# Optimization experiments

Measured on AMD Instinct MI355X. Metric: run time of the kernel, lower is better.

## Reference

```python
import jax, jax.numpy as jnp
import numpy as np
import math

N, D, C = 1024, 512, 70722
M_MARGIN = 0.4
H_SCALE = 0.333
S_SCALE = 64.0
EPS = 0.001


def setup_inputs() -> dict:
    key = jax.random.key(0)
    k1, k2, k3 = jax.random.split(key, 3)
    x = jax.random.normal(k1, (N, D), dtype=jnp.float32)
    labels = jax.random.randint(k2, (N,), 0, C, dtype=jnp.int64)
    # weights ~ N(0, 0.01) as in nn.Parameter init
    weights = 0.01 * jax.random.normal(k3, (C, D), dtype=jnp.float32)
    return {"x": x, "labels": labels, "weights": weights}


def reference(x, labels, weights):
    # world_size == 1: all-gather is identity and all labels are local.
    x_norms = jnp.maximum(jnp.linalg.norm(x, axis=1, keepdims=True), 1e-8)  # [N,1]

    norm_emb = x / jnp.maximum(jnp.linalg.norm(x, axis=1, keepdims=True), 1e-12)
    norm_w = weights / jnp.maximum(jnp.linalg.norm(weights, axis=1, keepdims=True), 1e-12)
    cosine = jnp.clip(norm_emb @ norm_w.T, -1.0, 1.0)  # [N,C]

    # AdaFace adaptive margin scaler (detached norms; t_alpha=1 -> batch stats = current stats)
    safe_norms = jax.lax.stop_gradient(jnp.clip(x_norms, 0.001, 100.0))  # [N,1]
    batch_mean = jnp.mean(safe_norms)
    batch_std = jnp.std(safe_norms, ddof=1)  # torch .std() is unbiased
    margin_scaler = jnp.clip((safe_norms - batch_mean) / (batch_std + EPS) * H_SCALE, -1.0, 1.0)  # [N,1]

    g_angular = -M_MARGIN * margin_scaler           # [N,1]
    g_add = M_MARGIN + M_MARGIN * margin_scaler     # [N,1]

    onehot = jax.nn.one_hot(labels, C, dtype=cosine.dtype)  # [N,C]

    theta = jnp.arccos(cosine)
    theta_m = jnp.clip(theta + onehot * g_angular, EPS, math.pi - EPS)
    logits = (jnp.cos(theta_m) - onehot * g_add) * S_SCALE  # [N,C]

    logp = jax.nn.log_softmax(logits, axis=-1)
    loss = -jnp.mean(jnp.take_along_axis(logp, labels[:, None], axis=1))
    return loss
```

## Files before the change

### kernel.cpp

```cpp
#include <hip/hip_runtime.h>
#include <hip/hip_bf16.h>
#include <stdint.h>

#define DIM 512
#define NROWS 1024
#define NCLS 70722

typedef float floatx4 __attribute__((ext_vector_type(4)));

__device__ __forceinline__ unsigned pk4_fp8(float a, float b, float c, float d) {
    unsigned v = 0;
    v = __builtin_amdgcn_cvt_pk_fp8_f32(a, b, v, false);
    v = __builtin_amdgcn_cvt_pk_fp8_f32(c, d, v, true);
    return v;
}

__device__ __forceinline__ float wave_reduce_sum(float s) {
    #pragma unroll
    for (int m = 1; m < 64; m <<= 1) s += __shfl_xor(s, m);
    return s;
}

__global__ __launch_bounds__(256) void prep_kernel(
        const float* __restrict__ x, const float* __restrict__ W,
        const int* __restrict__ labels,
        uint8_t* __restrict__ An, uint8_t* __restrict__ Wn8,
        float* __restrict__ rownorm, float* __restrict__ coslab,
        float* __restrict__ rowsum) {
    int b = blockIdx.x;
    int wv = threadIdx.x >> 6, lane = threadIdx.x & 63;
    if (b < NROWS / 4) {
        if (threadIdx.x < 4) rowsum[b * 4 + threadIdx.x] = 0.0f;
        int row = b * 4 + wv;
        int lab = labels[row];
        const float4* xs = (const float4*)(x + (size_t)row * DIM);
        const float4* ws = (const float4*)(W + (size_t)lab * DIM);
        float4 xa = xs[lane * 2], xb = xs[lane * 2 + 1];
        float4 wa = ws[lane * 2], wb = ws[lane * 2 + 1];
        float dxx = xa.x*xa.x + xa.y*xa.y + xa.z*xa.z + xa.w*xa.w
                  + xb.x*xb.x + xb.y*xb.y + xb.z*xb.z + xb.w*xb.w;
        float dww = wa.x*wa.x + wa.y*wa.y + wa.z*wa.z + wa.w*wa.w
                  + wb.x*wb.x + wb.y*wb.y + wb.z*wb.z + wb.w*wb.w;
        float dxw = xa.x*wa.x + xa.y*wa.y + xa.z*wa.z + xa.w*wa.w
                  + xb.x*wb.x + xb.y*wb.y + xb.z*wb.z + xb.w*wb.w;
        dxx = wave_reduce_sum(dxx);
        dww = wave_reduce_sum(dww);
        dxw = wave_reduce_sum(dxw);
        float norm = sqrtf(dxx);
        float s16 = 16.0f / fmaxf(norm, 1e-12f);
        uint2 p;
        p.x = pk4_fp8(xa.x*s16, xa.y*s16, xa.z*s16, xa.w*s16);
        p.y = pk4_fp8(xb.x*s16, xb.y*s16, xb.z*s16, xb.w*s16);
        *(uint2*)(An + (size_t)row * DIM + lane * 8) = p;
        if (lane == 0) {
            rownorm[row] = norm;
            coslab[row]  = dxw / (fmaxf(norm, 1e-12f) * fmaxf(sqrtf(dww), 1e-12f));
        }
    } else {
        int c = (b - NROWS / 4) * 4 + wv;
        if (c < NCLS) {
            const float4* src = (const float4*)(W + (size_t)c * DIM);
            float4 va = src[lane * 2], vb = src[lane * 2 + 1];
            float ss = va.x*va.x + va.y*va.y + va.z*va.z + va.w*va.w
                     + vb.x*vb.x + vb.y*vb.y + vb.z*vb.z + vb.w*vb.w;
            ss = wave_reduce_sum(ss);
            float s16 = 16.0f / fmaxf(sqrtf(ss), 1e-12f);
            uint2 p;
            p.x = pk4_fp8(va.x*s16, va.y*s16, va.z*s16, va.w*s16);
            p.y = pk4_fp8(vb.x*s16, vb.y*s16, vb.z*s16, vb.w*s16);
            *(uint2*)(Wn8 + (size_t)c * DIM + lane * 8) = p;
        }
    }
}

__global__ __launch_bounds__(512, 2) void gemm6_kernel(
        const uint8_t* __restrict__ An, const uint8_t* __restrict__ Wn8,
        float* __restrict__ rowsum) {
    __shared__ uint8_t Asm[128 * 512];
    __shared__ uint8_t Bsm[2][256 * 128];
    __shared__ float red[128];

    int b = blockIdx.x;
    int mgrp = b >> 5, cgrp = b & 31;
    int tid = threadIdx.x, lane = tid & 63, wv = tid >> 6;
    if (tid < 128) red[tid] = 0.0f;

    int arow = tid >> 5;
    int aq = ((tid & 31) ^ (arow & 7)) * 16;
    const uint8_t* aGb = An + (size_t)(mgrp * 128 + arow) * DIM + aq;

    int brow = lane >> 3;
    int ckB = ((lane & 7) ^ brow) * 16;

    int wm = (wv >> 2) * 64, wn = (wv & 3) * 64;
    int fr = lane & 15, fq = lane >> 4;
    int fh = fq >> 1, fl = (fq & 1) * 8;

    const floatx4 vzero = {0.0f, 0.0f, 0.0f, 0.0f};
    floatx4 acc[4][4] = {};

#define GLL(gp, lp) __builtin_amdgcn_global_load_lds( \
        (const __attribute__((address_space(1))) unsigned int*)(gp), \
        (__attribute__((address_space(3))) unsigned int*)(lp), 16, 0, 0)
#define BAR  __builtin_amdgcn_s_barrier()
#define FEN  asm volatile("" ::: "memory")

    #pragma unroll
    for (int i = 0; i < 8; ++i)
        GLL(aGb + i * 8192, Asm + i * 8192 + wv * 1024);

    const uint8_t *bp0, *bp1, *bp2, *bp3;
    {
        int cb = cgrp * 256 + wv * 32 + brow;
        bp0 = Wn8 + (size_t)min(cb,      NCLS - 1) * DIM + ckB;
        bp1 = Wn8 + (size_t)min(cb + 8,  NCLS - 1) * DIM + ckB;
        bp2 = Wn8 + (size_t)min(cb + 16, NCLS - 1) * DIM + ckB;
        bp3 = Wn8 + (size_t)min(cb + 24, NCLS - 1) * DIM + ckB;
    }

#define STAGE_B(slot, kb) do { \
        uint8_t* _d = Bsm[slot] + wv * 4096; \
        GLL(bp0 + (kb), _d); \
        GLL(bp1 + (kb), _d + 1024); \
        GLL(bp2 + (kb), _d + 2048); \
        GLL(bp3 + (kb), _d + 3072); } while (0)

#define COMPUTE(slot, cA) do { \
        long af[4][4], bg[4][4]; \
        _Pragma("unroll") \
        for (int m = 0; m < 4; ++m) { \
            int R = wm + m * 16 + fr; \
            const uint8_t* rp = Asm + R * 512 + fl; \
            _Pragma("unroll") \
            for (int ks = 0; ks < 4; ++ks) { \
                int cch = (cA) + ks * 2 + fh; \
                af[m][ks] = *(const long*)(rp + ((cch ^ (R & 7)) * 16)); \
            } \
        } \
        _Pragma("unroll") \
        for (int n = 0; n < 4; ++n) { \
            int R = wn + n * 16 + fr; \
            const uint8_t* rp = Bsm[slot] + R * 128 + fl; \
            _Pragma("unroll") \
            for (int ks = 0; ks < 4; ++ks) { \
                int cch = ks * 2 + fh; \
                bg[n][ks] = *(const long*)(rp + ((cch ^ (R & 7)) * 16)); \
            } \
        } \
        _Pragma("unroll") \
        for (int ks = 0; ks < 4; ++ks) \
            _Pragma("unroll") \
            for (int m = 0; m < 4; ++m) \
                _Pragma("unroll") \
                for (int n = 0; n < 4; ++n) \
                    acc[m][n] = __builtin_amdgcn_mfma_f32_16x16x32_fp8_fp8( \
                        af[m][ks], bg[n][ks], acc[m][n], 0, 0, 0); \
    } while (0)

    STAGE_B(0, 0);

    int nct = (cgrp < 21) ? 9 : 8;
    int c = cgrp;
    for (int ct = 0; ct < nct; ++ct) {
        STAGE_B(1, 128);
        asm volatile("s_waitcnt vmcnt(4)" ::: "memory");
        BAR;
        COMPUTE(0, 0);
        FEN; BAR;
        STAGE_B(0, 256);
        asm volatile("s_waitcnt vmcnt(4)" ::: "memory");
        BAR;
        COMPUTE(1, 8);
        FEN; BAR;
        STAGE_B(1, 384);
        asm volatile("s_waitcnt vmcnt(4)" ::: "memory");
        BAR;
        COMPUTE(0, 16);
        FEN; BAR;
        if (ct != nct - 1) {
            int cb = (c + 32) * 256 + wv * 32 + brow;
            bp0 = Wn8 + (size_t)min(cb,      NCLS - 1) * DIM + ckB;
            bp1 = Wn8 + (size_t)min(cb + 8,  NCLS - 1) * DIM + ckB;
            bp2 = Wn8 + (size_t)min(cb + 16, NCLS - 1) * DIM + ckB;
            bp3 = Wn8 + (size_t)min(cb + 24, NCLS - 1) * DIM + ckB;
            STAGE_B(0, 0);
            asm volatile("s_waitcnt vmcnt(4)" ::: "memory");
        } else {
            asm volatile("s_waitcnt vmcnt(0)" ::: "memory");
        }
        BAR;
        COMPUTE(1, 24);
        FEN; BAR;

        {
            const float CLIPC = 0.99999950f;
            const float ISCL  = 1.0f / 256.0f;
            int colbase = c * 256 + wn + fr;
            #pragma unroll
            for (int m = 0; m < 4; ++m) {
                #pragma unroll
                for (int reg = 0; reg < 4; ++reg) {
                    float s = 0.0f;
                    #pragma unroll
                    for (int n = 0; n < 4; ++n) {
                        int col = colbase + n * 16;
                        float cc = acc[m][n][reg] * ISCL;
                        cc = fminf(fmaxf(cc, -CLIPC), CLIPC);
                        float term = __expf(64.0f * cc - 64.0f);
                        s += (col < NCLS) ? term : 0.0f;
                    }
                    s += __shfl_xor(s, 1); s += __shfl_xor(s, 2);
                    s += __shfl_xor(s, 4); s += __shfl_xor(s, 8);
                    if (fr == 0) atomicAdd(&red[wm + m * 16 + fq * 4 + reg], s);
                }
            }
            #pragma unroll
            for (int m = 0; m < 4; ++m)
                #pragma unroll
                for (int n = 0; n < 4; ++n)
                    acc[m][n] = vzero;
        }
        c += 32;
    }

#undef GLL
#undef STAGE_B
#undef COMPUTE
#undef BAR
#undef FEN

    __syncthreads();
    if (tid < 128) atomicAdd(rowsum + mgrp * 128 + tid, red[tid]);
}

__global__ __launch_bounds__(1024) void finalize_kernel(
        const float* __restrict__ rowsum, const float* __restrict__ coslab,
        const float* __restrict__ rownorm, float* __restrict__ out) {
    __shared__ float sd[1024];
    int t = threadIdx.x;
    float v = fminf(fmaxf(rownorm[t], 0.001f), 100.0f);
    sd[t] = v; __syncthreads();
    for (int s = 512; s > 0; s >>= 1) { if (t < s) sd[t] += sd[t + s]; __syncthreads(); }
    float mean = sd[0] * (1.0f / 1024.0f);
    __syncthreads();
    float d = v - mean;
    sd[t] = d * d; __syncthreads();
    for (int s = 512; s > 0; s >>= 1) { if (t < s) sd[t] += sd[t + s]; __syncthreads(); }
    float stdv = sqrtf(sd[0] * (1.0f / 1023.0f));
    float ms = d / (stdv + 0.001f) * 0.333f;
    ms = fminf(fmaxf(ms, -1.0f), 1.0f);
    float g_ang = -0.4f * ms;
    float g_add =  0.4f + 0.4f * ms;
    const float CLIPC = 0.99999950f;
    const float PI = 3.14159265358979323846f;
    float cl  = fminf(fmaxf(coslab[t], -1.0f), 1.0f);
    float cne = fminf(fmaxf(cl, -CLIPC), CLIPC);
    float logit_non = 64.0f * cne;
    float theta = acosf(cl);
    float tm = fminf(fmaxf(theta + g_ang, 0.001f), PI - 0.001f);
    float logit_true = (__cosf(tm) - g_add) * 64.0f;
    float ssum = rowsum[t] - __expf(logit_non - 64.0f) + __expf(logit_true - 64.0f);
    float loss = logf(ssum) + 64.0f - logit_true;
    __syncthreads();
    sd[t] = loss; __syncthreads();
    for (int s = 512; s > 0; s >>= 1) { if (t < s) sd[t] += sd[t + s]; __syncthreads(); }
    if (t == 0) out[0] = sd[0] * (1.0f / 1024.0f);
}

extern "C" void kernel_launch(void* const* d_in, const int* in_sizes, int n_in,
                              void* d_out, int out_size, void* d_ws, size_t ws_size,
                              hipStream_t stream) {
    const float* x      = (const float*)d_in[0];
    const int*   labels = (const int*)d_in[1];
    const float* W      = (const float*)d_in[2];
    float* out = (float*)d_out;
    char* ws = (char*)d_ws;

    const size_t SZ_WN8 = 36212736;
    const size_t SZ_AN  = 524288;
    uint8_t* Wn8 = (uint8_t*)ws;
    uint8_t* An  = (uint8_t*)(ws + SZ_WN8);
    float* rownorm = (float*)(ws + SZ_WN8 + SZ_AN);
    float* rowsum  = rownorm + 1024;
    float* coslab  = rowsum + 1024;

    int wblocks = (NCLS + 3) / 4;
    prep_kernel<<<NROWS / 4 + wblocks, 256, 0, stream>>>(
        x, W, labels, An, Wn8, rownorm, coslab, rowsum);
    gemm6_kernel<<<256, 512, 0, stream>>>(An, Wn8, rowsum);
    finalize_kernel<<<1, 1024, 0, stream>>>(rowsum, coslab, rownorm, out);
}
```

Baseline: 299.3 us.

## Hold A fragments in registers, defer row-sum reductions, add MFMA priority

The GEMM now loads every A-operand fragment for the wave's 64 rows once into registers (64 longs) rather than re-reading them from LDS in each K sub-step. The per-tile shuffle-and-atomic row reduction is replaced by per-thread running sums that are reduced once at the end. MFMA sections are wrapped in s_setprio to favour compute waves. The finalize kernel switches from a shared-memory tree reduction to wave shuffles. The larger register footprint risks spills or reduced occupancy under the 512x2 launch bound.

```diff
diff --git a/kernel.cpp b/kernel.cpp
--- a/kernel.cpp
+++ b/kernel.cpp
@@ -73,7 +73,7 @@
     }
 }
 
-__global__ __launch_bounds__(512, 2) void gemm6_kernel(
+__global__ __launch_bounds__(512, 2) void gemm7_kernel(
         const uint8_t* __restrict__ An, const uint8_t* __restrict__ Wn8,
         float* __restrict__ rowsum) {
     __shared__ uint8_t Asm[128 * 512];
@@ -98,6 +98,8 @@
 
     const floatx4 vzero = {0.0f, 0.0f, 0.0f, 0.0f};
     floatx4 acc[4][4] = {};
+    float srun[4][4] = {};
+    long af[4][16];
 
 #define GLL(gp, lp) __builtin_amdgcn_global_load_lds( \
         (const __attribute__((address_space(1))) unsigned int*)(gp), \
@@ -125,39 +127,36 @@
         GLL(bp2 + (kb), _d + 2048); \
         GLL(bp3 + (kb), _d + 3072); } while (0)
 
-#define COMPUTE(slot, cA) do { \
-        long af[4][4], bg[4][4]; \
-        _Pragma("unroll") \
-        for (int m = 0; m < 4; ++m) { \
-            int R = wm + m * 16 + fr; \
-            const uint8_t* rp = Asm + R * 512 + fl; \
-            _Pragma("unroll") \
-            for (int ks = 0; ks < 4; ++ks) { \
-                int cch = (cA) + ks * 2 + fh; \
-                af[m][ks] = *(const long*)(rp + ((cch ^ (R & 7)) * 16)); \
-            } \
-        } \
+    STAGE_B(0, 0);
+    asm volatile("s_waitcnt vmcnt(4)" ::: "memory");
+    BAR;
+
+    #pragma unroll
+    for (int m = 0; m < 4; ++m) {
+        int R = wm + m * 16 + fr;
+        const uint8_t* rp = Asm + R * 512 + fl;
+        #pragma unroll
+        for (int ksl = 0; ksl < 16; ++ksl)
+            af[m][ksl] = *(const long*)(rp + (((2 * ksl + fh) ^ (R & 7)) * 16));
+    }
+
+#define COMPUTE(slot, KSB) do { \
         _Pragma("unroll") \
         for (int n = 0; n < 4; ++n) { \
             int R = wn + n * 16 + fr; \
             const uint8_t* rp = Bsm[slot] + R * 128 + fl; \
+            long bg[4]; \
             _Pragma("unroll") \
-            for (int ks = 0; ks < 4; ++ks) { \
-                int cch = ks * 2 + fh; \
-                bg[n][ks] = *(const long*)(rp + ((cch ^ (R & 7)) * 16)); \
-            } \
+            for (int ks = 0; ks < 4; ++ks) \
+                bg[ks] = *(const long*)(rp + (((ks * 2 + fh) ^ (R & 7)) * 16)); \
+            _Pragma("unroll") \
+            for (int ks = 0; ks < 4; ++ks) \
+                _Pragma("unroll") \
+                for (int m = 0; m < 4; ++m) \
+                    acc[m][n] = __builtin_amdgcn_mfma_f32_16x16x32_fp8_fp8( \
+                        af[m][(KSB) + ks], bg[ks], acc[m][n], 0, 0, 0); \
         } \
-        _Pragma("unroll") \
-        for (int ks = 0; ks < 4; ++ks) \
-            _Pragma("unroll") \
-            for (int m = 0; m < 4; ++m) \
-                _Pragma("unroll") \
-                for (int n = 0; n < 4; ++n) \
-                    acc[m][n] = __builtin_amdgcn_mfma_f32_16x16x32_fp8_fp8( \
-                        af[m][ks], bg[n][ks], acc[m][n], 0, 0, 0); \
     } while (0)
-
-    STAGE_B(0, 0);
 
     int nct = (cgrp < 21) ? 9 : 8;
     int c = cgrp;
@@ -165,17 +164,17 @@
         STAGE_B(1, 128);
         asm volatile("s_waitcnt vmcnt(4)" ::: "memory");
         BAR;
-        COMPUTE(0, 0);
+        __builtin_amdgcn_s_setprio(1); COMPUTE(0, 0);  __builtin_amdgcn_s_setprio(0);
         FEN; BAR;
         STAGE_B(0, 256);
         asm volatile("s_waitcnt vmcnt(4)" ::: "memory");
         BAR;
-        COMPUTE(1, 8);
+        __builtin_amdgcn_s_setprio(1); COMPUTE(1, 4);  __builtin_amdgcn_s_setprio(0);
         FEN; BAR;
         STAGE_B(1, 384);
         asm volatile("s_waitcnt vmcnt(4)" ::: "memory");
         BAR;
-        COMPUTE(0, 16);
+        __builtin_amdgcn_s_setprio(1); COMPUTE(0, 8);  __builtin_amdgcn_s_setprio(0);
         FEN; BAR;
         if (ct != nct - 1) {
             int cb = (c + 32) * 256 + wv * 32 + brow;
@@ -189,7 +188,7 @@
             asm volatile("s_waitcnt vmcnt(0)" ::: "memory");
         }
         BAR;
-        COMPUTE(1, 24);
+        __builtin_amdgcn_s_setprio(1); COMPUTE(1, 12); __builtin_amdgcn_s_setprio(0);
         FEN; BAR;
 
         {
@@ -209,9 +208,7 @@
                         float term = __expf(64.0f * cc - 64.0f);
                         s += (col < NCLS) ? term : 0.0f;
                     }
-                    s += __shfl_xor(s, 1); s += __shfl_xor(s, 2);
-                    s += __shfl_xor(s, 4); s += __shfl_xor(s, 8);
-                    if (fr == 0) atomicAdd(&red[wm + m * 16 + fq * 4 + reg], s);
+                    srun[m][reg] += s;
                 }
             }
             #pragma unroll
@@ -229,6 +226,16 @@
 #undef BAR
 #undef FEN
 
+    #pragma unroll
+    for (int m = 0; m < 4; ++m) {
+        #pragma unroll
+        for (int reg = 0; reg < 4; ++reg) {
+            float s = srun[m][reg];
+            s += __shfl_xor(s, 1); s += __shfl_xor(s, 2);
+            s += __shfl_xor(s, 4); s += __shfl_xor(s, 8);
+            if (fr == 0) atomicAdd(&red[wm + m * 16 + fq * 4 + reg], s);
+        }
+    }
     __syncthreads();
     if (tid < 128) atomicAdd(rowsum + mgrp * 128 + tid, red[tid]);
 }
@@ -236,17 +243,34 @@
 __global__ __launch_bounds__(1024) void finalize_kernel(
         const float* __restrict__ rowsum, const float* __restrict__ coslab,
         const float* __restrict__ rownorm, float* __restrict__ out) {
-    __shared__ float sd[1024];
-    int t = threadIdx.x;
+    __shared__ float part[16];
+    __shared__ float bc[2];
+    int t = threadIdx.x, lane = t & 63, w = t >> 6;
     float v = fminf(fmaxf(rownorm[t], 0.001f), 100.0f);
-    sd[t] = v; __syncthreads();
-    for (int s = 512; s > 0; s >>= 1) { if (t < s) sd[t] += sd[t + s]; __syncthreads(); }
-    float mean = sd[0] * (1.0f / 1024.0f);
-    __syncthreads();
+
+    float s = wave_reduce_sum(v);
+    if (lane == 0) part[w] = s;
+    __syncthreads();
+    if (t < 64) {
+        float p = (lane < 16) ? part[lane] : 0.0f;
+        p = wave_reduce_sum(p);
+        if (lane == 0) bc[0] = p * (1.0f / 1024.0f);
+    }
+    __syncthreads();
+    float mean = bc[0];
     float d = v - mean;
-    sd[t] = d * d; __syncthreads();
-    for (int s = 512; s > 0; s >>= 1) { if (t < s) sd[t] += sd[t + s]; __syncthreads(); }
-    float stdv = sqrtf(sd[0] * (1.0f / 1023.0f));
+
+    s = wave_reduce_sum(d * d);
+    if (lane == 0) part[w] = s;
+    __syncthreads();
+    if (t < 64) {
+        float p = (lane < 16) ? part[lane] : 0.0f;
+        p = wave_reduce_sum(p);
+        if (lane == 0) bc[1] = sqrtf(p * (1.0f / 1023.0f));
+    }
+    __syncthreads();
+    float stdv = bc[1];
+
     float ms = d / (stdv + 0.001f) * 0.333f;
     ms = fminf(fmaxf(ms, -1.0f), 1.0f);
     float g_ang = -0.4f * ms;
@@ -261,10 +285,15 @@
     float logit_true = (__cosf(tm) - g_add) * 64.0f;
     float ssum = rowsum[t] - __expf(logit_non - 64.0f) + __expf(logit_true - 64.0f);
     float loss = logf(ssum) + 64.0f - logit_true;
-    __syncthreads();
-    sd[t] = loss; __syncthreads();
-    for (int s = 512; s > 0; s >>= 1) { if (t < s) sd[t] += sd[t + s]; __syncthreads(); }
-    if (t == 0) out[0] = sd[0] * (1.0f / 1024.0f);
+
+    s = wave_reduce_sum(loss);
+    if (lane == 0) part[w] = s;
+    __syncthreads();
+    if (t < 64) {
+        float p = (lane < 16) ? part[lane] : 0.0f;
+        p = wave_reduce_sum(p);
+        if (lane == 0) out[0] = p * (1.0f / 1024.0f);
+    }
 }
 
 extern "C" void kernel_launch(void* const* d_in, const int* in_sizes, int n_in,
@@ -287,6 +316,6 @@
     int wblocks = (NCLS + 3) / 4;
     prep_kernel<<<NROWS / 4 + wblocks, 256, 0, stream>>>(
         x, W, labels, An, Wn8, rownorm, coslab, rowsum);
-    gemm6_kernel<<<256, 512, 0, stream>>>(An, Wn8, rowsum);
+    gemm7_kernel<<<256, 512, 0, stream>>>(An, Wn8, rowsum);
     finalize_kernel<<<1, 1024, 0, stream>>>(rowsum, coslab, rownorm, out);
 }
```

Result: faster. 292.1 us (-2.4%).
